# Kernel optimization log

Hardware: AMD Instinct MI355X
Metric: run time of the kernel (lower is better)

## Reference

```python
import jax, jax.numpy as jnp
import numpy as np

N, IN_F, HID, HEADS, OUT_F, E, G = 20000, 256, 128, 4, 10, 400000, 64
HC = HID * HEADS  # 512


def gatv2_layer(x, src, dst, Wl, bl, Wr, br, att, bias, num_nodes):
    # PyG GATv2Conv (concat=True): lin_l for source msgs, lin_r for targets
    H, C = att.shape
    xl = (x @ Wl + bl).reshape(-1, H, C)
    xr = (x @ Wr + br).reshape(-1, H, C)
    # edge-wise GATv2 score: a^T LeakyReLU(xl_j + xr_i)
    e = jax.nn.leaky_relu(xl[src] + xr[dst], 0.2)          # [E,H,C]
    logits = jnp.einsum('ehc,hc->eh', e, att)              # [E,H]
    # segment softmax over incoming edges of each destination node
    m = jax.ops.segment_max(logits, dst, num_segments=num_nodes)
    p = jnp.exp(logits - m[dst])
    denom = jax.ops.segment_sum(p, dst, num_segments=num_nodes)
    alpha = p / denom[dst]                                 # [E,H]
    out = jax.ops.segment_sum(alpha[:, :, None] * xl[src], dst,
                              num_segments=num_nodes)      # [N,H,C]
    return out.reshape(num_nodes, H * C) + bias


def setup_inputs() -> dict:
    key = jax.random.key(0)
    ks = jax.random.split(key, 32)
    s = 0.05
    inp = {
        'x': jax.random.normal(ks[0], (N, IN_F), jnp.float32),
        'edge_index': jax.random.randint(ks[1], (2, E), 0, N, jnp.int64),
        'batch': jnp.sort(jax.random.randint(ks[2], (N,), 0, G, jnp.int64)),
        'pre_W': jax.random.normal(ks[3], (IN_F, HID), jnp.float32) * s,
        'pre_b': jnp.zeros((HID,), jnp.float32),
        'cls_W': jax.random.normal(ks[4], (HC, OUT_F), jnp.float32) * s,
        'cls_b': jnp.zeros((OUT_F,), jnp.float32),
    }
    in_dims = [HID, HC, HC]
    for i in range(3):
        kk = jax.random.split(ks[5 + i], 6)
        d = in_dims[i]
        inp[f'Wl{i+1}'] = jax.random.normal(kk[0], (d, HC), jnp.float32) * s
        inp[f'bl{i+1}'] = jnp.zeros((HC,), jnp.float32)
        inp[f'Wr{i+1}'] = jax.random.normal(kk[1], (d, HC), jnp.float32) * s
        inp[f'br{i+1}'] = jnp.zeros((HC,), jnp.float32)
        inp[f'att{i+1}'] = jax.random.normal(kk[2], (HEADS, HID), jnp.float32) * s
        inp[f'bias{i+1}'] = jnp.zeros((HC,), jnp.float32)
    return inp


def reference(x, edge_index, batch, pre_W, pre_b, cls_W, cls_b,
              Wl1, bl1, Wr1, br1, att1, bias1,
              Wl2, bl2, Wr2, br2, att2, bias2,
              Wl3, bl3, Wr3, br3, att3, bias3):
    num_nodes = x.shape[0]
    # add self loops (PyG GATv2Conv default)
    loop = jnp.arange(num_nodes, dtype=edge_index.dtype)
    src = jnp.concatenate([edge_index[0], loop])
    dst = jnp.concatenate([edge_index[1], loop])

    h = jax.nn.elu(x @ pre_W + pre_b)  # dropout is identity in eval
    h = jax.nn.elu(gatv2_layer(h, src, dst, Wl1, bl1, Wr1, br1, att1, bias1, num_nodes))
    h = jax.nn.elu(gatv2_layer(h, src, dst, Wl2, bl2, Wr2, br2, att2, bias2, num_nodes))
    h = jax.nn.elu(gatv2_layer(h, src, dst, Wl3, bl3, Wr3, br3, att3, bias3, num_nodes))
    # global mean pool over graphs
    sums = jax.ops.segment_sum(h, batch, num_segments=G)
    cnts = jax.ops.segment_sum(jnp.ones((num_nodes,), h.dtype), batch, num_segments=G)
    pooled = sums / jnp.maximum(cnts, 1.0)[:, None]
    return pooled @ cls_W + cls_b
```

## Files before the change

kernel.cpp:

```cpp
#include <hip/hip_runtime.h>
#include <hip/hip_bf16.h>
#include <math.h>

#define NODES   20000
#define MPAD    20096
#define IN_F    256
#define HID     128
#define HEADS   4
#define OUT_F   10
#define NEDGE   400000
#define NGRAPH  64
#define HC      512
#define EPRIME  (NEDGE + NODES)
#define XLRW    1024

typedef __attribute__((ext_vector_type(8))) short bf16x8_t;
typedef __attribute__((ext_vector_type(4))) float f32x4_t;

__device__ __forceinline__ float2 pk_add(float2 a, float2 b) {
    float2 d;
    asm("v_pk_add_f32 %0, %1, %2" : "=v"(d) : "v"(a), "v"(b));
    return d;
}
__device__ __forceinline__ float2 pk_mul(float2 a, float2 b) {
    float2 d;
    asm("v_pk_mul_f32 %0, %1, %2" : "=v"(d) : "v"(a), "v"(b));
    return d;
}
__device__ __forceinline__ float2 pk_fma(float2 a, float2 b, float2 c) {
    float2 d;
    asm("v_pk_fma_f32 %0, %1, %2, %3" : "=v"(d) : "v"(a), "v"(b), "v"(c));
    return d;
}
__device__ __forceinline__ float2 abs2(float2 s) {
    float2 r;
    r.x = __uint_as_float(__float_as_uint(s.x) & 0x7fffffffu);
    r.y = __uint_as_float(__float_as_uint(s.y) & 0x7fffffffu);
    return r;
}

__device__ __forceinline__ unsigned short bf16_rne(float f) {
    unsigned int u = __float_as_uint(f);
    u += 0x7FFFu + ((u >> 16) & 1u);
    return (unsigned short)(u >> 16);
}
__device__ __forceinline__ float bf16f(unsigned short h) {
    return __uint_as_float(((unsigned int)h) << 16);
}
__device__ __forceinline__ void split2(float f, unsigned short& hi, unsigned short& lo) {
    hi = bf16_rne(f);
    lo = bf16_rne(f - bf16f(hi));
}

#define GLOAD_LDS16(gp, lp) \
    __builtin_amdgcn_global_load_lds((const __attribute__((address_space(1))) unsigned int*)(gp), \
                                     (__attribute__((address_space(3))) unsigned int*)(lp), 16, 0, 0)

__global__ __launch_bounds__(256) void hist_kernel(const int* __restrict__ ei,
                                                   int* __restrict__ counts) {
    int e = blockIdx.x * blockDim.x + threadIdx.x;
    if (e >= EPRIME) return;
    int dst = (e < NEDGE) ? ei[NEDGE + e] : (e - NEDGE);
    atomicAdd(&counts[dst], 1);
}

__global__ __launch_bounds__(1024) void scan_kernel(const int* __restrict__ counts,
                                                    int* __restrict__ offsets,
                                                    int* __restrict__ cursor) {
    __shared__ int wsum[16];
    __shared__ int s_carry;
    const int tid = threadIdx.x;
    const int lane = tid & 63, wid = tid >> 6;
    if (tid == 0) s_carry = 0;
    __syncthreads();
    for (int base = 0; base < NODES; base += 1024) {
        int idx = base + tid;
        int v = (idx < NODES) ? counts[idx] : 0;
        int x = v;
        #pragma unroll
        for (int d = 1; d < 64; d <<= 1) {
            int n = __shfl_up(x, d);
            if (lane >= d) x += n;
        }
        if (lane == 63) wsum[wid] = x;
        __syncthreads();
        if (wid == 0) {
            int w = (lane < 16) ? wsum[lane] : 0;
            #pragma unroll
            for (int d = 1; d < 16; d <<= 1) {
                int n = __shfl_up(w, d);
                if (lane >= d) w += n;
            }
            if (lane < 16) wsum[lane] = w;
        }
        __syncthreads();
        int carry = s_carry;
        int wpre = (wid == 0) ? 0 : wsum[wid - 1];
        int excl = carry + wpre + x - v;
        if (idx < NODES) { offsets[idx] = excl; cursor[idx] = excl; }
        __syncthreads();
        if (tid == 1023) s_carry = carry + wsum[15];
        __syncthreads();
    }
    if (tid == 0) offsets[NODES] = s_carry;
}

__global__ __launch_bounds__(256) void scatter_kernel(const int* __restrict__ ei,
                                                      int* __restrict__ cursor,
                                                      int* __restrict__ srcsb) {
    int e = blockIdx.x * blockDim.x + threadIdx.x;
    if (e >= EPRIME) return;
    int src, dst;
    if (e < NEDGE) { src = ei[e]; dst = ei[NEDGE + e]; }
    else           { src = dst = e - NEDGE; }
    int pos = atomicAdd(&cursor[dst], 1);
    srcsb[pos] = src << 12;
}

__global__ __launch_bounds__(256) void convert_x_kernel(const float* __restrict__ x,
                                                        unsigned short* __restrict__ x2) {
    int idx = blockIdx.x * 256 + threadIdx.x;
    int r = idx >> 5, g = idx & 31;
    if (r >= MPAD) return;
    __align__(16) unsigned short hv[8], lv[8];
    if (r < NODES) {
        const float* p = &x[(size_t)r * IN_F + g * 8];
        #pragma unroll
        for (int j = 0; j < 8; ++j) split2(p[j], hv[j], lv[j]);
    } else {
        #pragma unroll
        for (int j = 0; j < 8; ++j) { hv[j] = 0; lv[j] = 0; }
    }
    unsigned short* o = x2 + (size_t)r * (2 * IN_F) + g * 16;
    *reinterpret_cast<uint4*>(o)     = *reinterpret_cast<uint4*>(hv);
    *reinterpret_cast<uint4*>(o + 8) = *reinterpret_cast<uint4*>(lv);
}

__global__ __launch_bounds__(256) void convert_w_kernel(const float* __restrict__ W,
                                                        unsigned short* __restrict__ WT2,
                                                        int K, int N, int gshift) {
    int idx = blockIdx.x * 256 + threadIdx.x;
    int n = idx >> gshift, g = idx & ((1 << gshift) - 1);
    if (n >= N) return;
    __align__(16) unsigned short hv[8], lv[8];
    #pragma unroll
    for (int j = 0; j < 8; ++j) split2(W[(size_t)(8 * g + j) * N + n], hv[j], lv[j]);
    unsigned short* o = WT2 + (size_t)n * (2 * K) + g * 16;
    *reinterpret_cast<uint4*>(o)     = *reinterpret_cast<uint4*>(hv);
    *reinterpret_cast<uint4*>(o + 8) = *reinterpret_cast<uint4*>(lv);
}

__global__ __launch_bounds__(256) void build_bias_kernel(const float* __restrict__ bl1,
                                                         const float* __restrict__ br1,
                                                         const float* __restrict__ bl2,
                                                         const float* __restrict__ br2,
                                                         const float* __restrict__ bl3,
                                                         const float* __restrict__ br3,
                                                         float* __restrict__ out) {
    int idx = blockIdx.x * 256 + threadIdx.x;
    if (idx >= 3 * 1024) return;
    int l = idx >> 10, c = idx & 1023;
    const float* p = (l == 0) ? (c < 512 ? bl1 : br1)
                   : (l == 1) ? (c < 512 ? bl2 : br2)
                              : (c < 512 ? bl3 : br3);
    out[idx] = p[c & 511];
}

template <int WRITE_SPLIT, int ACT>
__global__ __launch_bounds__(256) void mfma_gemm_kernel(const unsigned short* __restrict__ A2,
                                                        const unsigned short* __restrict__ B2,
                                                        const float* __restrict__ bias,
                                                        float* __restrict__ Cf,
                                                        unsigned short* __restrict__ C2,
                                                        int M, int N, int K) {
    __shared__ char lds[32768];
    const int tid = threadIdx.x;
    const int w = tid >> 6, l = tid & 63;
    const int wr = w >> 1, wc = w & 1;
    const int row0 = blockIdx.x * 128, col0 = blockIdx.y * 128;
    const size_t rowB = (size_t)K * 4;

    f32x4_t acc[4][4];
    #pragma unroll
    for (int i = 0; i < 4; ++i)
        #pragma unroll
        for (int j = 0; j < 4; ++j)
            #pragma unroll
            for (int q = 0; q < 4; ++q) acc[i][j][q] = 0.f;

    const int ssub = l >> 3;
    const int scol = (l & 7) * 16;
    const int g16  = l >> 4;
    const int fr   = l & 15;

    const char* Ab = (const char*)A2;
    const char* Bb = (const char*)B2;

    const int nsteps = K >> 5;
    for (int t = 0; t < nsteps; ++t) {
        #pragma unroll
        for (int i = 0; i < 4; ++i) {
            int r = w * 32 + i * 8 + ssub;
            size_t gb = (size_t)(row0 + r) * rowB + (size_t)t * 128 + (size_t)(scol ^ ((r & 7) << 4));
            GLOAD_LDS16(Ab + gb, &lds[(w * 32 + i * 8) * 128]);
        }
        #pragma unroll
        for (int i = 0; i < 4; ++i) {
            int r = w * 32 + i * 8 + ssub;
            size_t gb = (size_t)(col0 + r) * rowB + (size_t)t * 128 + (size_t)(scol ^ ((r & 7) << 4));
            GLOAD_LDS16(Bb + gb, &lds[16384 + (w * 32 + i * 8) * 128]);
        }
        asm volatile("s_waitcnt vmcnt(0)" ::: "memory");
        __syncthreads();

        bf16x8_t ah[4], al[4];
        #pragma unroll
        for (int i = 0; i < 4; ++i) {
            int r = wr * 64 + i * 16 + fr;
            int sw = (r & 7) << 4;
            ah[i] = *reinterpret_cast<const bf16x8_t*>(&lds[r * 128 + ((g16 * 32) ^ sw)]);
            al[i] = *reinterpret_cast<const bf16x8_t*>(&lds[r * 128 + ((g16 * 32 + 16) ^ sw)]);
        }
        #pragma unroll
        for (int j = 0; j < 4; ++j) {
            int r = wc * 64 + j * 16 + fr;
            int sw = (r & 7) << 4;
            bf16x8_t bh = *reinterpret_cast<const bf16x8_t*>(&lds[16384 + r * 128 + ((g16 * 32) ^ sw)]);
            bf16x8_t bl = *reinterpret_cast<const bf16x8_t*>(&lds[16384 + r * 128 + ((g16 * 32 + 16) ^ sw)]);
            #pragma unroll
            for (int i = 0; i < 4; ++i) {
                acc[i][j] = __builtin_amdgcn_mfma_f32_16x16x32_bf16(ah[i], bh, acc[i][j], 0, 0, 0);
                acc[i][j] = __builtin_amdgcn_mfma_f32_16x16x32_bf16(ah[i], bl, acc[i][j], 0, 0, 0);
                acc[i][j] = __builtin_amdgcn_mfma_f32_16x16x32_bf16(al[i], bh, acc[i][j], 0, 0, 0);
            }
        }
        __syncthreads();
    }

    const int crb  = (l >> 4) * 4;
    const int ccol = l & 15;
    #pragma unroll
    for (int i = 0; i < 4; ++i) {
        #pragma unroll
        for (int jj = 0; jj < 4; ++jj) {
            int rg = row0 + wr * 64 + i * 16 + crb + jj;
            #pragma unroll
            for (int j = 0; j < 4; ++j) {
                int cg = col0 + wc * 64 + j * 16 + ccol;
                float v = acc[i][j][jj] + bias[cg];
                if (ACT) v = v > 0.f ? v : expm1f(v);
                if (WRITE_SPLIT) {
                    unsigned short hi, lo;
                    split2(v, hi, lo);
                    unsigned short* o = C2 + (size_t)rg * (2 * N) + (cg >> 3) * 16 + (cg & 7);
                    o[0] = hi; o[8] = lo;
                } else {
                    if (rg < M) Cf[(size_t)rg * N + cg] = v;
                }
            }
        }
    }
}

__global__ __launch_bounds__(128) void gat_edge_kernel(const float* __restrict__ xlr,
                                                       const float* __restrict__ att,
                                                       const float* __restrict__ bias,
                                                       const int* __restrict__ offsets,
                                                       const int* __restrict__ srcsb,
                                                       unsigned short* __restrict__ h2) {
    const int node = blockIdx.x;
    if (node >= NODES) {
        ((uint4*)(h2 + (size_t)node * (2 * HC)))[threadIdx.x] = make_uint4(0u, 0u, 0u, 0u);
        return;
    }
    const int tid = threadIdx.x;
    const int head = tid >> 5;
    const int hl   = tid & 31;
    const int wl   = tid & 63;
    const int ch0  = head * HID + hl * 4;
    const char* xlb = (const char*)xlr;
    const int laneoff = ch0 * 4;

    const float4 atv = *reinterpret_cast<const float4*>(&att[ch0]);
    const float L2E = 1.44269504f;
    const float2 a6p0 = make_float2(0.6f * L2E * atv.x, 0.6f * L2E * atv.y);
    const float2 a6p1 = make_float2(0.6f * L2E * atv.z, 0.6f * L2E * atv.w);
    const float2 a4p0 = make_float2(0.4f * L2E * atv.x, 0.4f * L2E * atv.y);
    const float2 a4p1 = make_float2(0.4f * L2E * atv.z, 0.4f * L2E * atv.w);
    const float4 xrv = *reinterpret_cast<const float4*>(&xlr[(size_t)node * XLRW + 512 + ch0]);
    const float2 xrp0 = make_float2(xrv.x, xrv.y);
    const float2 xrp1 = make_float2(xrv.z, xrv.w);

    const int ibase = ((wl & 32) + (wl & 7)) << 2;
    const int idx0 = ibase, idx1 = ibase + (8 << 2);
    const int idx2 = ibase + (16 << 2), idx3 = ibase + (24 << 2);

    const int beg = offsets[node], end = offsets[node + 1];
    const bool b4 = (hl & 16) != 0, b3 = (hl & 8) != 0;

    float m = -INFINITY, denom = 0.f;
    float a0 = 0.f, a1 = 0.f, a2 = 0.f, a3 = 0.f;

    for (int e0 = beg; e0 < end; e0 += 4) {
        const int nb = min(4, end - e0);
        int sb[4]; float4 xv[4]; float p[4];
        #pragma unroll
        for (int q = 0; q < 4; ++q) sb[q] = srcsb[e0 + ((q < nb) ? q : nb - 1)];
        #pragma unroll
        for (int q = 0; q < 4; ++q)
            xv[q] = *reinterpret_cast<const float4*>(xlb + (size_t)(unsigned)sb[q] + laneoff);
        #pragma unroll
        for (int q = 0; q < 4; ++q) {
            float2 s0 = pk_add(make_float2(xv[q].x, xv[q].y), xrp0);
            float2 s1 = pk_add(make_float2(xv[q].z, xv[q].w), xrp1);
            float2 pp = pk_mul(a6p0, s0);
            pp = pk_fma(a4p0, abs2(s0), pp);
            pp = pk_fma(a6p1, s1, pp);
            pp = pk_fma(a4p1, abs2(s1), pp);
            p[q] = pp.x + pp.y;
        }
        float s0 = b4 ? p[0] : p[2];
        float u0 = (b4 ? p[2] : p[0]) + __shfl_xor(s0, 16);
        float s1 = b4 ? p[1] : p[3];
        float u1 = (b4 ? p[3] : p[1]) + __shfl_xor(s1, 16);
        float s2 = b3 ? u0 : u1;
        float t  = (b3 ? u1 : u0) + __shfl_xor(s2, 8);
        t += __shfl_xor(t, 4);
        t += __shfl_xor(t, 2);
        t += __shfl_xor(t, 1);
        const int ti = __float_as_int(t);
        const float pe0 = __int_as_float(__builtin_amdgcn_ds_bpermute(idx0, ti));
        const float pe1 = __int_as_float(__builtin_amdgcn_ds_bpermute(idx1, ti));
        const float pe2 = __int_as_float(__builtin_amdgcn_ds_bpermute(idx2, ti));
        const float pe3 = __int_as_float(__builtin_amdgcn_ds_bpermute(idx3, ti));

        const float m4 = fmaxf(fmaxf(pe0, pe1), fmaxf(pe2, pe3));
        if (m4 > m) {
            float sc = exp2f(m - m4);
            denom *= sc; a0 *= sc; a1 *= sc; a2 *= sc; a3 *= sc;
            m = m4;
        }
        {
            float w0 = exp2f(pe0 - m);
            denom += w0;
            a0 = fmaf(w0, xv[0].x, a0); a1 = fmaf(w0, xv[0].y, a1);
            a2 = fmaf(w0, xv[0].z, a2); a3 = fmaf(w0, xv[0].w, a3);
        }
        if (nb > 1) {
            float w1 = exp2f(pe1 - m);
            denom += w1;
            a0 = fmaf(w1, xv[1].x, a0); a1 = fmaf(w1, xv[1].y, a1);
            a2 = fmaf(w1, xv[1].z, a2); a3 = fmaf(w1, xv[1].w, a3);
        }
        if (nb > 2) {
            float w2 = exp2f(pe2 - m);
            denom += w2;
            a0 = fmaf(w2, xv[2].x, a0); a1 = fmaf(w2, xv[2].y, a1);
            a2 = fmaf(w2, xv[2].z, a2); a3 = fmaf(w2, xv[2].w, a3);
        }
        if (nb > 3) {
            float w3 = exp2f(pe3 - m);
            denom += w3;
            a0 = fmaf(w3, xv[3].x, a0); a1 = fmaf(w3, xv[3].y, a1);
            a2 = fmaf(w3, xv[3].z, a2); a3 = fmaf(w3, xv[3].w, a3);
        }
    }

    const float inv = 1.f / denom;
    const float4 bv = *reinterpret_cast<const float4*>(&bias[ch0]);
    float o0 = a0 * inv + bv.x, o1 = a1 * inv + bv.y;
    float o2 = a2 * inv + bv.z, o3 = a3 * inv + bv.w;
    o0 = o0 > 0.f ? o0 : expm1f(o0);
    o1 = o1 > 0.f ? o1 : expm1f(o1);
    o2 = o2 > 0.f ? o2 : expm1f(o2);
    o3 = o3 > 0.f ? o3 : expm1f(o3);
    __align__(8) unsigned short hv[4], lv[4];
    split2(o0, hv[0], lv[0]); split2(o1, hv[1], lv[1]);
    split2(o2, hv[2], lv[2]); split2(o3, hv[3], lv[3]);
    unsigned short* o = h2 + (size_t)node * (2 * HC) + ((ch0 >> 3) * 16) + (ch0 & 7);
    *reinterpret_cast<uint2*>(o)     = *reinterpret_cast<uint2*>(hv);
    *reinterpret_cast<uint2*>(o + 8) = *reinterpret_cast<uint2*>(lv);
}

__global__ __launch_bounds__(256) void pool_part_kernel(const unsigned short* __restrict__ h2,
                                                        const int* __restrict__ batch,
                                                        float* __restrict__ partial) {
    const int g = blockIdx.x, part = blockIdx.y;
    int lo = 0, hi = NODES;
    while (lo < hi) { int mid = (lo + hi) >> 1; if (batch[mid] < g) lo = mid + 1; else hi = mid; }
    const int s = lo;
    lo = s; hi = NODES;
    while (lo < hi) { int mid = (lo + hi) >> 1; if (batch[mid] < g + 1) lo = mid + 1; else hi = mid; }
    const int e = lo, cnt = e - s;
    const int ps = s + (cnt * part) / 4;
    const int pe = s + (cnt * (part + 1)) / 4;

    const int c0 = threadIdx.x * 2;
    const int boff = ((c0 >> 3) * 16) + (c0 & 7);
    float s0 = 0.f, s1 = 0.f;
    for (int r = ps; r < pe; ++r) {
        const unsigned short* p = h2 + (size_t)r * (2 * HC) + boff;
        s0 += bf16f(p[0]) + bf16f(p[8]);
        s1 += bf16f(p[1]) + bf16f(p[9]);
    }
    float* o = partial + ((size_t)(g * 4 + part)) * HC;
    o[c0] = s0; o[c0 + 1] = s1;
}

__global__ __launch_bounds__(256) void cls_kernel(const float* __restrict__ partial,
                                                  const int* __restrict__ batch,
                                                  const float* __restrict__ W,
                                                  const float* __restrict__ cb,
                                                  float* __restrict__ outp) {
    const int g = blockIdx.x;
    __shared__ float pooled[HC];
    int lo = 0, hi = NODES;
    while (lo < hi) { int mid = (lo + hi) >> 1; if (batch[mid] < g) lo = mid + 1; else hi = mid; }
    const int s = lo;
    lo = s; hi = NODES;
    while (lo < hi) { int mid = (lo + hi) >> 1; if (batch[mid] < g + 1) lo = mid + 1; else hi = mid; }
    const int cnt = lo - s;

    const int c0 = threadIdx.x * 2;
    float s0 = 0.f, s1 = 0.f;
    #pragma unroll
    for (int part = 0; part < 4; ++part) {
        const float* p = partial + ((size_t)(g * 4 + part)) * HC;
        s0 += p[c0]; s1 += p[c0 + 1];
    }
    const float invc = cnt > 0 ? 1.f / (float)cnt : 0.f;
    pooled[c0] = s0 * invc; pooled[c0 + 1] = s1 * invc;
    __syncthreads();

    const int lane = threadIdx.x & 63, wid = threadIdx.x >> 6;
    for (int o = wid; o < OUT_F; o += 4) {
        float p = 0.f;
        for (int c = lane; c < HC; c += 64) p += pooled[c] * W[c * OUT_F + o];
        #pragma unroll
        for (int off2 = 32; off2; off2 >>= 1) p += __shfl_xor(p, off2);
        if (lane == 0) outp[g * OUT_F + o] = p + cb[o];
    }
}

extern "C" void kernel_launch(void* const* d_in, const int* in_sizes, int n_in,
                              void* d_out, int out_size, void* d_ws, size_t ws_size,
                              hipStream_t stream) {
    const float* x      = (const float*)d_in[0];
    const int*   ei     = (const int*)d_in[1];
    const int*   batch  = (const int*)d_in[2];
    const float* pre_W  = (const float*)d_in[3];
    const float* pre_b  = (const float*)d_in[4];
    const float* cls_W  = (const float*)d_in[5];
    const float* cls_b  = (const float*)d_in[6];
    const float* Wl[3]; const float* bl[3]; const float* Wr[3];
    const float* br[3]; const float* attw[3]; const float* bw[3];
    for (int l = 0; l < 3; ++l) {
        Wl[l]   = (const float*)d_in[7 + 6 * l + 0];
        bl[l]   = (const float*)d_in[7 + 6 * l + 1];
        Wr[l]   = (const float*)d_in[7 + 6 * l + 2];
        br[l]   = (const float*)d_in[7 + 6 * l + 3];
        attw[l] = (const float*)d_in[7 + 6 * l + 4];
        bw[l]   = (const float*)d_in[7 + 6 * l + 5];
    }
    float* outp = (float*)d_out;

    char* ws = (char*)d_ws;
    size_t off = 0;
    auto alloc = [&](size_t b) { char* p = ws + off; off += (b + 255) & ~(size_t)255; return p; };
    float* xlr = (float*)alloc((size_t)MPAD * XLRW * 4);
    unsigned short* h2 = (unsigned short*)alloc((size_t)MPAD * 2 * HC * 2);
    unsigned short* WT2f = (unsigned short*)alloc((size_t)1024 * 2 * HC * 2);
    unsigned short* preWT2 = (unsigned short*)alloc((size_t)HID * 2 * IN_F * 2);
    float* biascat = (float*)alloc(3 * 1024 * 4);
    int* counts  = (int*)alloc(NODES * 4);
    int* offsets = (int*)alloc((NODES + 1) * 4);
    int* cursor  = (int*)alloc(NODES * 4);
    int* srcsb   = (int*)alloc((size_t)EPRIME * 4);
    unsigned short* x2 = (unsigned short*)xlr;
    float* partial = xlr;

    hipMemsetAsync(counts, 0, NODES * 4, stream);
    hist_kernel<<<(EPRIME + 255) / 256, 256, 0, stream>>>(ei, counts);
    scan_kernel<<<1, 1024, 0, stream>>>(counts, offsets, cursor);
    scatter_kernel<<<(EPRIME + 255) / 256, 256, 0, stream>>>(ei, cursor, srcsb);

    convert_x_kernel<<<(MPAD * (IN_F / 8) + 255) / 256, 256, 0, stream>>>(x, x2);
    convert_w_kernel<<<(HID * (IN_F / 8) + 255) / 256, 256, 0, stream>>>(pre_W, preWT2, IN_F, HID, 5);
    build_bias_kernel<<<12, 256, 0, stream>>>(bl[0], br[0], bl[1], br[1], bl[2], br[2], biascat);
    convert_w_kernel<<<(HC * (HID / 8) + 255) / 256, 256, 0, stream>>>(Wl[0], WT2f, HID, HC, 4);
    convert_w_kernel<<<(HC * (HID / 8) + 255) / 256, 256, 0, stream>>>(Wr[0], WT2f + (size_t)512 * 2 * HID, HID, HC, 4);

    mfma_gemm_kernel<1, 1><<<dim3(157, 1), 256, 0, stream>>>(x2, preWT2, pre_b,
                                                             nullptr, h2, NODES, HID, IN_F);

    mfma_gemm_kernel<0, 0><<<dim3(157, 8), 256, 0, stream>>>(h2, WT2f, biascat, xlr, nullptr, NODES, 1024, HID);
    convert_w_kernel<<<(HC * (HC / 8) + 255) / 256, 256, 0, stream>>>(Wl[1], WT2f, HC, HC, 6);
    convert_w_kernel<<<(HC * (HC / 8) + 255) / 256, 256, 0, stream>>>(Wr[1], WT2f + (size_t)512 * 2 * HC, HC, HC, 6);
    gat_edge_kernel<<<MPAD, 128, 0, stream>>>(xlr, attw[0], bw[0], offsets, srcsb, h2);

    mfma_gemm_kernel<0, 0><<<dim3(157, 8), 256, 0, stream>>>(h2, WT2f, biascat + 1024, xlr, nullptr, NODES, 1024, HC);
    convert_w_kernel<<<(HC * (HC / 8) + 255) / 256, 256, 0, stream>>>(Wl[2], WT2f, HC, HC, 6);
    convert_w_kernel<<<(HC * (HC / 8) + 255) / 256, 256, 0, stream>>>(Wr[2], WT2f + (size_t)512 * 2 * HC, HC, HC, 6);
    gat_edge_kernel<<<MPAD, 128, 0, stream>>>(xlr, attw[1], bw[1], offsets, srcsb, h2);

    mfma_gemm_kernel<0, 0><<<dim3(157, 8), 256, 0, stream>>>(h2, WT2f, biascat + 2048, xlr, nullptr, NODES, 1024, HC);
    gat_edge_kernel<<<MPAD, 128, 0, stream>>>(xlr, attw[2], bw[2], offsets, srcsb, h2);

    pool_part_kernel<<<dim3(NGRAPH, 4), 256, 0, stream>>>(h2, batch, partial);
    cls_kernel<<<NGRAPH, 256, 0, stream>>>(partial, batch, cls_W, cls_b, outp);
}
```

Before: 830.9 us.

## Software-pipeline GAT edge gathers in batches of eight, two nodes per block

The edge aggregation kernel now handles edges in batches of eight instead of four. It prefetches the next batch's source indices and feature rows while it computes the current batch's scores, and it widens the shuffle-reduction tree to eight edges per pass. Blocks grow to 256 threads and cover two nodes each, which halves the grid. The aim is to hide gather latency and cut per-edge shuffle overhead, at the cost of many more registers (two sets of eight float4s), which may reduce occupancy.

Result: no change. 821.8 us (-1.1%).

```diff
diff --git a/kernel.cpp b/kernel.cpp
--- a/kernel.cpp
+++ b/kernel.cpp
@@ -262,20 +262,22 @@
     }
 }
 
-__global__ __launch_bounds__(128) void gat_edge_kernel(const float* __restrict__ xlr,
+__global__ __launch_bounds__(256) void gat_edge_kernel(const float* __restrict__ xlr,
                                                        const float* __restrict__ att,
                                                        const float* __restrict__ bias,
                                                        const int* __restrict__ offsets,
                                                        const int* __restrict__ srcsb,
                                                        unsigned short* __restrict__ h2) {
-    const int node = blockIdx.x;
+    const int tid = threadIdx.x;
+    const int grp = tid >> 7;
+    const int node = blockIdx.x * 2 + grp;
+    const int t = tid & 127;
     if (node >= NODES) {
-        ((uint4*)(h2 + (size_t)node * (2 * HC)))[threadIdx.x] = make_uint4(0u, 0u, 0u, 0u);
+        ((uint4*)(h2 + (size_t)node * (2 * HC)))[t] = make_uint4(0u, 0u, 0u, 0u);
         return;
     }
-    const int tid = threadIdx.x;
-    const int head = tid >> 5;
-    const int hl   = tid & 31;
+    const int head = t >> 5;
+    const int hl   = t & 31;
     const int wl   = tid & 63;
     const int ch0  = head * HID + hl * 4;
     const char* xlb = (const char*)xlr;
@@ -291,26 +293,40 @@
     const float2 xrp0 = make_float2(xrv.x, xrv.y);
     const float2 xrp1 = make_float2(xrv.z, xrv.w);
 
-    const int ibase = ((wl & 32) + (wl & 7)) << 2;
-    const int idx0 = ibase, idx1 = ibase + (8 << 2);
-    const int idx2 = ibase + (16 << 2), idx3 = ibase + (24 << 2);
+    const int ibase = ((wl & 32) | (wl & 3)) << 2;
 
     const int beg = offsets[node], end = offsets[node + 1];
-    const bool b4 = (hl & 16) != 0, b3 = (hl & 8) != 0;
+    const bool b4 = (hl & 16) != 0, b3 = (hl & 8) != 0, b2 = (hl & 4) != 0;
 
     float m = -INFINITY, denom = 0.f;
     float a0 = 0.f, a1 = 0.f, a2 = 0.f, a3 = 0.f;
 
-    for (int e0 = beg; e0 < end; e0 += 4) {
-        const int nb = min(4, end - e0);
-        int sb[4]; float4 xv[4]; float p[4];
-        #pragma unroll
-        for (int q = 0; q < 4; ++q) sb[q] = srcsb[e0 + ((q < nb) ? q : nb - 1)];
-        #pragma unroll
-        for (int q = 0; q < 4; ++q)
-            xv[q] = *reinterpret_cast<const float4*>(xlb + (size_t)(unsigned)sb[q] + laneoff);
-        #pragma unroll
-        for (int q = 0; q < 4; ++q) {
+    int e0 = beg;
+    int nb = min(8, end - beg);
+    int sb[8]; float4 xv[8];
+    #pragma unroll
+    for (int q = 0; q < 8; ++q) sb[q] = srcsb[e0 + ((q < nb) ? q : nb - 1)];
+    #pragma unroll
+    for (int q = 0; q < 8; ++q)
+        xv[q] = *reinterpret_cast<const float4*>(xlb + (size_t)(unsigned)sb[q] + laneoff);
+
+    while (true) {
+        const int e1 = e0 + 8;
+        const bool more = e1 < end;
+        int nbn = 0;
+        int sbn[8]; float4 xvn[8];
+        if (more) {
+            nbn = min(8, end - e1);
+            #pragma unroll
+            for (int q = 0; q < 8; ++q) sbn[q] = srcsb[e1 + ((q < nbn) ? q : nbn - 1)];
+            #pragma unroll
+            for (int q = 0; q < 8; ++q)
+                xvn[q] = *reinterpret_cast<const float4*>(xlb + (size_t)(unsigned)sbn[q] + laneoff);
+        }
+
+        float p[8];
+        #pragma unroll
+        for (int q = 0; q < 8; ++q) {
             float2 s0 = pk_add(make_float2(xv[q].x, xv[q].y), xrp0);
             float2 s1 = pk_add(make_float2(xv[q].z, xv[q].w), xrp1);
             float2 pp = pk_mul(a6p0, s0);
@@ -319,51 +335,45 @@
             pp = pk_fma(a4p1, abs2(s1), pp);
             p[q] = pp.x + pp.y;
         }
-        float s0 = b4 ? p[0] : p[2];
-        float u0 = (b4 ? p[2] : p[0]) + __shfl_xor(s0, 16);
-        float s1 = b4 ? p[1] : p[3];
-        float u1 = (b4 ? p[3] : p[1]) + __shfl_xor(s1, 16);
-        float s2 = b3 ? u0 : u1;
-        float t  = (b3 ? u1 : u0) + __shfl_xor(s2, 8);
-        t += __shfl_xor(t, 4);
-        t += __shfl_xor(t, 2);
-        t += __shfl_xor(t, 1);
-        const int ti = __float_as_int(t);
-        const float pe0 = __int_as_float(__builtin_amdgcn_ds_bpermute(idx0, ti));
-        const float pe1 = __int_as_float(__builtin_amdgcn_ds_bpermute(idx1, ti));
-        const float pe2 = __int_as_float(__builtin_amdgcn_ds_bpermute(idx2, ti));
-        const float pe3 = __int_as_float(__builtin_amdgcn_ds_bpermute(idx3, ti));
-
-        const float m4 = fmaxf(fmaxf(pe0, pe1), fmaxf(pe2, pe3));
-        if (m4 > m) {
-            float sc = exp2f(m - m4);
+        float u[4];
+        #pragma unroll
+        for (int q = 0; q < 4; ++q) {
+            float s = b4 ? p[q] : p[q + 4];
+            u[q] = (b4 ? p[q + 4] : p[q]) + __shfl_xor(s, 16);
+        }
+        float v0, v1;
+        { float s = b3 ? u[0] : u[2]; v0 = (b3 ? u[2] : u[0]) + __shfl_xor(s, 8); }
+        { float s = b3 ? u[1] : u[3]; v1 = (b3 ? u[3] : u[1]) + __shfl_xor(s, 8); }
+        float tt;
+        { float s = b2 ? v0 : v1; tt = (b2 ? v1 : v0) + __shfl_xor(s, 4); }
+        tt += __shfl_xor(tt, 2);
+        tt += __shfl_xor(tt, 1);
+        const int ti = __float_as_int(tt);
+        float pe[8];
+        #pragma unroll
+        for (int q = 0; q < 8; ++q)
+            pe[q] = __int_as_float(__builtin_amdgcn_ds_bpermute(ibase + (q << 4), ti));
+
+        const float m8 = fmaxf(fmaxf(fmaxf(pe[0], pe[1]), fmaxf(pe[2], pe[3])),
+                               fmaxf(fmaxf(pe[4], pe[5]), fmaxf(pe[6], pe[7])));
+        if (m8 > m) {
+            float sc = exp2f(m - m8);
             denom *= sc; a0 *= sc; a1 *= sc; a2 *= sc; a3 *= sc;
-            m = m4;
-        }
-        {
-            float w0 = exp2f(pe0 - m);
-            denom += w0;
-            a0 = fmaf(w0, xv[0].x, a0); a1 = fmaf(w0, xv[0].y, a1);
-            a2 = fmaf(w0, xv[0].z, a2); a3 = fmaf(w0, xv[0].w, a3);
-        }
-        if (nb > 1) {
-            float w1 = exp2f(pe1 - m);
-            denom += w1;
-            a0 = fmaf(w1, xv[1].x, a0); a1 = fmaf(w1, xv[1].y, a1);
-            a2 = fmaf(w1, xv[1].z, a2); a3 = fmaf(w1, xv[1].w, a3);
-        }
-        if (nb > 2) {
-            float w2 = exp2f(pe2 - m);
-            denom += w2;
-            a0 = fmaf(w2, xv[2].x, a0); a1 = fmaf(w2, xv[2].y, a1);
-            a2 = fmaf(w2, xv[2].z, a2); a3 = fmaf(w2, xv[2].w, a3);
-        }
-        if (nb > 3) {
-            float w3 = exp2f(pe3 - m);
-            denom += w3;
-            a0 = fmaf(w3, xv[3].x, a0); a1 = fmaf(w3, xv[3].y, a1);
-            a2 = fmaf(w3, xv[3].z, a2); a3 = fmaf(w3, xv[3].w, a3);
-        }
+            m = m8;
+        }
+        #pragma unroll
+        for (int q = 0; q < 8; ++q) {
+            if (q >= nb) break;
+            float wq = exp2f(pe[q] - m);
+            denom += wq;
+            a0 = fmaf(wq, xv[q].x, a0); a1 = fmaf(wq, xv[q].y, a1);
+            a2 = fmaf(wq, xv[q].z, a2); a3 = fmaf(wq, xv[q].w, a3);
+        }
+
+        if (!more) break;
+        #pragma unroll
+        for (int q = 0; q < 8; ++q) { sb[q] = sbn[q]; xv[q] = xvn[q]; }
+        nb = nbn; e0 = e1;
     }
 
     const float inv = 1.f / denom;
@@ -496,15 +506,15 @@
     mfma_gemm_kernel<0, 0><<<dim3(157, 8), 256, 0, stream>>>(h2, WT2f, biascat, xlr, nullptr, NODES, 1024, HID);
     convert_w_kernel<<<(HC * (HC / 8) + 255) / 256, 256, 0, stream>>>(Wl[1], WT2f, HC, HC, 6);
     convert_w_kernel<<<(HC * (HC / 8) + 255) / 256, 256, 0, stream>>>(Wr[1], WT2f + (size_t)512 * 2 * HC, HC, HC, 6);
-    gat_edge_kernel<<<MPAD, 128, 0, stream>>>(xlr, attw[0], bw[0], offsets, srcsb, h2);
+    gat_edge_kernel<<<MPAD / 2, 256, 0, stream>>>(xlr, attw[0], bw[0], offsets, srcsb, h2);
 
     mfma_gemm_kernel<0, 0><<<dim3(157, 8), 256, 0, stream>>>(h2, WT2f, biascat + 1024, xlr, nullptr, NODES, 1024, HC);
     convert_w_kernel<<<(HC * (HC / 8) + 255) / 256, 256, 0, stream>>>(Wl[2], WT2f, HC, HC, 6);
     convert_w_kernel<<<(HC * (HC / 8) + 255) / 256, 256, 0, stream>>>(Wr[2], WT2f + (size_t)512 * 2 * HC, HC, HC, 6);
-    gat_edge_kernel<<<MPAD, 128, 0, stream>>>(xlr, attw[1], bw[1], offsets, srcsb, h2);
+    gat_edge_kernel<<<MPAD / 2, 256, 0, stream>>>(xlr, attw[1], bw[1], offsets, srcsb, h2);
 
     mfma_gemm_kernel<0, 0><<<dim3(157, 8), 256, 0, stream>>>(h2, WT2f, biascat + 2048, xlr, nullptr, NODES, 1024, HC);
-    gat_edge_kernel<<<MPAD, 128, 0, stream>>>(xlr, attw[2], bw[2], offsets, srcsb, h2);
+    gat_edge_kernel<<<MPAD / 2, 256, 0, stream>>>(xlr, attw[2], bw[2], offsets, srcsb, h2);
 
     pool_part_kernel<<<dim3(NGRAPH, 4), 256, 0, stream>>>(h2, batch, partial);
     cls_kernel<<<NGRAPH, 256, 0, stream>>>(partial, batch, cls_W, cls_b, outp);
```

## Double-buffer gathered source features into LDS in GAT edge kernel

Applied to the files above, without the earlier changes.

The GAT edge aggregation now uses global_load_lds to prefetch the next batch of edge indices and gathered source rows into double-buffered shared memory, overlapping the gather with compute on the current batch. Each block handles two destination nodes with 256 threads, and accumulation uses packed float2 FMAs. The srcsb buffer is padded by 8 zeroed entries so index prefetches past the end stay in bounds. In exchange the kernel uses about 33KB of LDS per block, which may limit occupancy, and depends on hand-placed vmcnt waits being correct.

New measurement: 840.5 us. Within noise of the previous version (+1.2%).

```diff
diff --git a/kernel.cpp b/kernel.cpp
--- a/kernel.cpp
+++ b/kernel.cpp
@@ -55,6 +55,9 @@
 #define GLOAD_LDS16(gp, lp) \
     __builtin_amdgcn_global_load_lds((const __attribute__((address_space(1))) unsigned int*)(gp), \
                                      (__attribute__((address_space(3))) unsigned int*)(lp), 16, 0, 0)
+#define GLOAD_LDS4(gp, lp) \
+    __builtin_amdgcn_global_load_lds((const __attribute__((address_space(1))) unsigned int*)(gp), \
+                                     (__attribute__((address_space(3))) unsigned int*)(lp), 4, 0, 0)
 
 __global__ __launch_bounds__(256) void hist_kernel(const int* __restrict__ ei,
                                                    int* __restrict__ counts) {
@@ -109,7 +112,8 @@
                                                       int* __restrict__ cursor,
                                                       int* __restrict__ srcsb) {
     int e = blockIdx.x * blockDim.x + threadIdx.x;
-    if (e >= EPRIME) return;
+    if (e >= EPRIME + 8) return;
+    if (e >= EPRIME) { srcsb[e] = 0; return; }
     int src, dst;
     if (e < NEDGE) { src = ei[e]; dst = ei[NEDGE + e]; }
     else           { src = dst = e - NEDGE; }
@@ -262,24 +266,27 @@
     }
 }
 
-__global__ __launch_bounds__(128) void gat_edge_kernel(const float* __restrict__ xlr,
+__global__ __launch_bounds__(256) void gat_edge_kernel(const float* __restrict__ xlr,
                                                        const float* __restrict__ att,
                                                        const float* __restrict__ bias,
                                                        const int* __restrict__ offsets,
                                                        const int* __restrict__ srcsb,
                                                        unsigned short* __restrict__ h2) {
-    const int node = blockIdx.x;
+    __shared__ char lds[33792];
+    const int tid = threadIdx.x;
+    const int grp = tid >> 7;
+    const int node = blockIdx.x * 2 + grp;
+    const int t128 = tid & 127;
     if (node >= NODES) {
-        ((uint4*)(h2 + (size_t)node * (2 * HC)))[threadIdx.x] = make_uint4(0u, 0u, 0u, 0u);
+        ((uint4*)(h2 + (size_t)node * (2 * HC)))[t128] = make_uint4(0u, 0u, 0u, 0u);
         return;
     }
-    const int tid = threadIdx.x;
-    const int head = tid >> 5;
-    const int hl   = tid & 31;
-    const int wl   = tid & 63;
-    const int ch0  = head * HID + hl * 4;
+    const int hl = t128 & 31;
+    const int wl = tid & 63;
+    const int ch0 = (t128 >> 5) * HID + hl * 4;
     const char* xlb = (const char*)xlr;
-    const int laneoff = ch0 * 4;
+    const char* sb  = (const char*)srcsb;
+    const int byteoff = t128 * 16;
 
     const float4 atv = *reinterpret_cast<const float4*>(&att[ch0]);
     const float L2E = 1.44269504f;
@@ -290,86 +297,140 @@
     const float4 xrv = *reinterpret_cast<const float4*>(&xlr[(size_t)node * XLRW + 512 + ch0]);
     const float2 xrp0 = make_float2(xrv.x, xrv.y);
     const float2 xrp1 = make_float2(xrv.z, xrv.w);
-
-    const int ibase = ((wl & 32) + (wl & 7)) << 2;
-    const int idx0 = ibase, idx1 = ibase + (8 << 2);
-    const int idx2 = ibase + (16 << 2), idx3 = ibase + (24 << 2);
-
     const int beg = offsets[node], end = offsets[node + 1];
+    const int nt = (end - beg + 3) >> 2;
+
+    char* gbase = &lds[grp * 16384];
+    char* islot = &lds[32768 + grp * 512];
+    const int wavehalf = (t128 >> 6) * 1024;
+    const int l3 = (wl & 3) * 4;
+
     const bool b4 = (hl & 16) != 0, b3 = (hl & 8) != 0;
+    const int pbase = ((wl & 32) | (wl & 7)) << 2;
 
     float m = -INFINITY, denom = 0.f;
-    float a0 = 0.f, a1 = 0.f, a2 = 0.f, a3 = 0.f;
-
-    for (int e0 = beg; e0 < end; e0 += 4) {
+    float2 acc01 = make_float2(0.f, 0.f), acc23 = make_float2(0.f, 0.f);
+
+    GLOAD_LDS4(sb + (size_t)beg * 4 + l3, islot);
+    asm volatile("s_waitcnt vmcnt(0)" ::: "memory");
+    __builtin_amdgcn_sched_barrier(0);
+    {
+        int4 i0 = *reinterpret_cast<const int4*>(islot);
+        GLOAD_LDS4(sb + (size_t)((beg + 4 < end) ? beg + 4 : beg) * 4 + l3, islot + 256);
+        const int nb0 = min(4, end - beg);
+        int s0 = i0.x;
+        int s1 = (1 < nb0) ? i0.y : s0;
+        int s2 = (2 < nb0) ? i0.z : s0;
+        int s3 = (3 < nb0) ? i0.w : s0;
+        char* wb = gbase + wavehalf;
+        GLOAD_LDS16(xlb + (size_t)(unsigned)s0 + byteoff, wb);
+        GLOAD_LDS16(xlb + (size_t)(unsigned)s1 + byteoff, wb + 2048);
+        GLOAD_LDS16(xlb + (size_t)(unsigned)s2 + byteoff, wb + 4096);
+        GLOAD_LDS16(xlb + (size_t)(unsigned)s3 + byteoff, wb + 6144);
+    }
+
+    for (int t = 0; t < nt; ++t) {
+        const int e0 = beg + t * 4;
         const int nb = min(4, end - e0);
-        int sb[4]; float4 xv[4]; float p[4];
-        #pragma unroll
-        for (int q = 0; q < 4; ++q) sb[q] = srcsb[e0 + ((q < nb) ? q : nb - 1)];
+        const bool more = (t + 1 < nt);
+        asm volatile("s_waitcnt vmcnt(4)" ::: "memory");
+        __builtin_amdgcn_sched_barrier(0);
+        int4 nidx = *reinterpret_cast<const int4*>(islot + ((t + 1) & 1) * 256);
+        const int e2 = e0 + 8;
+        GLOAD_LDS4(sb + (size_t)((e2 < end) ? e2 : beg) * 4 + l3, islot + (t & 1) * 256);
+        if (more) {
+            const int nbn = min(4, end - (e0 + 4));
+            int s0 = nidx.x;
+            int s1 = (1 < nbn) ? nidx.y : s0;
+            int s2 = (2 < nbn) ? nidx.z : s0;
+            int s3 = (3 < nbn) ? nidx.w : s0;
+            char* wb = gbase + ((t + 1) & 1) * 8192 + wavehalf;
+            GLOAD_LDS16(xlb + (size_t)(unsigned)s0 + byteoff, wb);
+            GLOAD_LDS16(xlb + (size_t)(unsigned)s1 + byteoff, wb + 2048);
+            GLOAD_LDS16(xlb + (size_t)(unsigned)s2 + byteoff, wb + 4096);
+            GLOAD_LDS16(xlb + (size_t)(unsigned)s3 + byteoff, wb + 6144);
+            asm volatile("s_waitcnt vmcnt(5)" ::: "memory");
+        } else {
+            asm volatile("s_waitcnt vmcnt(1)" ::: "memory");
+        }
+        __builtin_amdgcn_sched_barrier(0);
+
+        const char* rb = gbase + (t & 1) * 8192;
+        float4 xv0 = *reinterpret_cast<const float4*>(rb + 0 * 2048 + byteoff);
+        float4 xv1 = *reinterpret_cast<const float4*>(rb + 1 * 2048 + byteoff);
+        float4 xv2 = *reinterpret_cast<const float4*>(rb + 2 * 2048 + byteoff);
+        float4 xv3 = *reinterpret_cast<const float4*>(rb + 3 * 2048 + byteoff);
+
+        float p[4];
+        {
+            float4 xq[4] = {xv0, xv1, xv2, xv3};
+            #pragma unroll
+            for (int q = 0; q < 4; ++q) {
+                float2 s0v = pk_add(make_float2(xq[q].x, xq[q].y), xrp0);
+                float2 s1v = pk_add(make_float2(xq[q].z, xq[q].w), xrp1);
+                float2 pp = pk_mul(a6p0, s0v);
+                pp = pk_fma(a4p0, abs2(s0v), pp);
+                pp = pk_fma(a6p1, s1v, pp);
+                pp = pk_fma(a4p1, abs2(s1v), pp);
+                p[q] = pp.x + pp.y;
+            }
+        }
+        float f0 = b4 ? p[0] : p[2];
+        float u0 = (b4 ? p[2] : p[0]) + __shfl_xor(f0, 16);
+        float f1 = b4 ? p[1] : p[3];
+        float u1 = (b4 ? p[3] : p[1]) + __shfl_xor(f1, 16);
+        float f2 = b3 ? u0 : u1;
+        float tt = (b3 ? u1 : u0) + __shfl_xor(f2, 8);
+        tt += __shfl_xor(tt, 4);
+        tt += __shfl_xor(tt, 2);
+        tt += __shfl_xor(tt, 1);
+        const int ti = __float_as_int(tt);
+        float pe[4];
         #pragma unroll
         for (int q = 0; q < 4; ++q)
-            xv[q] = *reinterpret_cast<const float4*>(xlb + (size_t)(unsigned)sb[q] + laneoff);
-        #pragma unroll
-        for (int q = 0; q < 4; ++q) {
-            float2 s0 = pk_add(make_float2(xv[q].x, xv[q].y), xrp0);
-            float2 s1 = pk_add(make_float2(xv[q].z, xv[q].w), xrp1);
-            float2 pp = pk_mul(a6p0, s0);
-            pp = pk_fma(a4p0, abs2(s0), pp);
-            pp = pk_fma(a6p1, s1, pp);
-            pp = pk_fma(a4p1, abs2(s1), pp);
-            p[q] = pp.x + pp.y;
-        }
-        float s0 = b4 ? p[0] : p[2];
-        float u0 = (b4 ? p[2] : p[0]) + __shfl_xor(s0, 16);
-        float s1 = b4 ? p[1] : p[3];
-        float u1 = (b4 ? p[3] : p[1]) + __shfl_xor(s1, 16);
-        float s2 = b3 ? u0 : u1;
-        float t  = (b3 ? u1 : u0) + __shfl_xor(s2, 8);
-        t += __shfl_xor(t, 4);
-        t += __shfl_xor(t, 2);
-        t += __shfl_xor(t, 1);
-        const int ti = __float_as_int(t);
-        const float pe0 = __int_as_float(__builtin_amdgcn_ds_bpermute(idx0, ti));
-        const float pe1 = __int_as_float(__builtin_amdgcn_ds_bpermute(idx1, ti));
-        const float pe2 = __int_as_float(__builtin_amdgcn_ds_bpermute(idx2, ti));
-        const float pe3 = __int_as_float(__builtin_amdgcn_ds_bpermute(idx3, ti));
-
-        const float m4 = fmaxf(fmaxf(pe0, pe1), fmaxf(pe2, pe3));
+            pe[q] = __int_as_float(__builtin_amdgcn_ds_bpermute(pbase + (q << 5), ti));
+
+        const float m4 = fmaxf(fmaxf(pe[0], pe[1]), fmaxf(pe[2], pe[3]));
         if (m4 > m) {
             float sc = exp2f(m - m4);
-            denom *= sc; a0 *= sc; a1 *= sc; a2 *= sc; a3 *= sc;
+            float2 sc2 = make_float2(sc, sc);
+            denom *= sc; acc01 = pk_mul(sc2, acc01); acc23 = pk_mul(sc2, acc23);
             m = m4;
         }
         {
-            float w0 = exp2f(pe0 - m);
-            denom += w0;
-            a0 = fmaf(w0, xv[0].x, a0); a1 = fmaf(w0, xv[0].y, a1);
-            a2 = fmaf(w0, xv[0].z, a2); a3 = fmaf(w0, xv[0].w, a3);
+            float wq = exp2f(pe[0] - m);
+            denom += wq;
+            float2 ww = make_float2(wq, wq);
+            acc01 = pk_fma(ww, make_float2(xv0.x, xv0.y), acc01);
+            acc23 = pk_fma(ww, make_float2(xv0.z, xv0.w), acc23);
         }
         if (nb > 1) {
-            float w1 = exp2f(pe1 - m);
-            denom += w1;
-            a0 = fmaf(w1, xv[1].x, a0); a1 = fmaf(w1, xv[1].y, a1);
-            a2 = fmaf(w1, xv[1].z, a2); a3 = fmaf(w1, xv[1].w, a3);
+            float wq = exp2f(pe[1] - m);
+            denom += wq;
+            float2 ww = make_float2(wq, wq);
+            acc01 = pk_fma(ww, make_float2(xv1.x, xv1.y), acc01);
+            acc23 = pk_fma(ww, make_float2(xv1.z, xv1.w), acc23);
         }
         if (nb > 2) {
-            float w2 = exp2f(pe2 - m);
-            denom += w2;
-            a0 = fmaf(w2, xv[2].x, a0); a1 = fmaf(w2, xv[2].y, a1);
-            a2 = fmaf(w2, xv[2].z, a2); a3 = fmaf(w2, xv[2].w, a3);
+            float wq = exp2f(pe[2] - m);
+            denom += wq;
+            float2 ww = make_float2(wq, wq);
+            acc01 = pk_fma(ww, make_float2(xv2.x, xv2.y), acc01);
+            acc23 = pk_fma(ww, make_float2(xv2.z, xv2.w), acc23);
         }
         if (nb > 3) {
-            float w3 = exp2f(pe3 - m);
-            denom += w3;
-            a0 = fmaf(w3, xv[3].x, a0); a1 = fmaf(w3, xv[3].y, a1);
-            a2 = fmaf(w3, xv[3].z, a2); a3 = fmaf(w3, xv[3].w, a3);
+            float wq = exp2f(pe[3] - m);
+            denom += wq;
+            float2 ww = make_float2(wq, wq);
+            acc01 = pk_fma(ww, make_float2(xv3.x, xv3.y), acc01);
+            acc23 = pk_fma(ww, make_float2(xv3.z, xv3.w), acc23);
         }
     }
 
     const float inv = 1.f / denom;
     const float4 bv = *reinterpret_cast<const float4*>(&bias[ch0]);
-    float o0 = a0 * inv + bv.x, o1 = a1 * inv + bv.y;
-    float o2 = a2 * inv + bv.z, o3 = a3 * inv + bv.w;
+    float o0 = acc01.x * inv + bv.x, o1 = acc01.y * inv + bv.y;
+    float o2 = acc23.x * inv + bv.z, o3 = acc23.y * inv + bv.w;
     o0 = o0 > 0.f ? o0 : expm1f(o0);
     o1 = o1 > 0.f ? o1 : expm1f(o1);
     o2 = o2 > 0.f ? o2 : expm1f(o2);
@@ -475,14 +536,14 @@
     int* counts  = (int*)alloc(NODES * 4);
     int* offsets = (int*)alloc((NODES + 1) * 4);
     int* cursor  = (int*)alloc(NODES * 4);
-    int* srcsb   = (int*)alloc((size_t)EPRIME * 4);
+    int* srcsb   = (int*)alloc((size_t)(EPRIME + 8) * 4);
     unsigned short* x2 = (unsigned short*)xlr;
     float* partial = xlr;
 
     hipMemsetAsync(counts, 0, NODES * 4, stream);
     hist_kernel<<<(EPRIME + 255) / 256, 256, 0, stream>>>(ei, counts);
     scan_kernel<<<1, 1024, 0, stream>>>(counts, offsets, cursor);
-    scatter_kernel<<<(EPRIME + 255) / 256, 256, 0, stream>>>(ei, cursor, srcsb);
+    scatter_kernel<<<(EPRIME + 8 + 255) / 256, 256, 0, stream>>>(ei, cursor, srcsb);
 
     convert_x_kernel<<<(MPAD * (IN_F / 8) + 255) / 256, 256, 0, stream>>>(x, x2);
     convert_w_kernel<<<(HID * (IN_F / 8) + 255) / 256, 256, 0, stream>>>(pre_W, preWT2, IN_F, HID, 5);
@@ -496,15 +557,15 @@
     mfma_gemm_kernel<0, 0><<<dim3(157, 8), 256, 0, stream>>>(h2, WT2f, biascat, xlr, nullptr, NODES, 1024, HID);
     convert_w_kernel<<<(HC * (HC / 8) + 255) / 256, 256, 0, stream>>>(Wl[1], WT2f, HC, HC, 6);
     convert_w_kernel<<<(HC * (HC / 8) + 255) / 256, 256, 0, stream>>>(Wr[1], WT2f + (size_t)512 * 2 * HC, HC, HC, 6);
-    gat_edge_kernel<<<MPAD, 128, 0, stream>>>(xlr, attw[0], bw[0], offsets, srcsb, h2);
+    gat_edge_kernel<<<MPAD / 2, 256, 0, stream>>>(xlr, attw[0], bw[0], offsets, srcsb, h2);
 
     mfma_gemm_kernel<0, 0><<<dim3(157, 8), 256, 0, stream>>>(h2, WT2f, biascat + 1024, xlr, nullptr, NODES, 1024, HC);
     convert_w_kernel<<<(HC * (HC / 8) + 255) / 256, 256, 0, stream>>>(Wl[2], WT2f, HC, HC, 6);
     convert_w_kernel<<<(HC * (HC / 8) + 255) / 256, 256, 0, stream>>>(Wr[2], WT2f + (size_t)512 * 2 * HC, HC, HC, 6);
-    gat_edge_kernel<<<MPAD, 128, 0, stream>>>(xlr, attw[1], bw[1], offsets, srcsb, h2);
+    gat_edge_kernel<<<MPAD / 2, 256, 0, stream>>>(xlr, attw[1], bw[1], offsets, srcsb, h2);
 
     mfma_gemm_kernel<0, 0><<<dim3(157, 8), 256, 0, stream>>>(h2, WT2f, biascat + 2048, xlr, nullptr, NODES, 1024, HC);
-    gat_edge_kernel<<<MPAD, 128, 0, stream>>>(xlr, attw[2], bw[2], offsets, srcsb, h2);
+    gat_edge_kernel<<<MPAD / 2, 256, 0, stream>>>(xlr, attw[2], bw[2], offsets, srcsb, h2);
 
     pool_part_kernel<<<dim3(NGRAPH, 4), 256, 0, stream>>>(h2, batch, partial);
     cls_kernel<<<NGRAPH, 256, 0, stream>>>(partial, batch, cls_W, cls_b, outp);
```
